# Kernel tuning notes

Hardware: AMD Instinct MI355X
Metric: run time of the kernel (lower is better)

Reference implementation:

```python
import jax, jax.numpy as jnp
import numpy as np

B, DIM, S, CS, H = 1024, 64, 256, 500, 128

def setup_inputs() -> dict:
    key = jax.random.key(0)
    ks = jax.random.split(key, 16)
    def rn(k, shape, scale=0.05):
        return jax.random.normal(k, shape, dtype=jnp.float32) * scale
    return {
        "x": rn(ks[0], (B, DIM, S - 1), 1.0),
        "snippet": jax.random.randint(ks[1], (B, DIM), 0, CS, dtype=jnp.int64),
        "snippet_list": rn(ks[2], (DIM, CS, S), 1.0),
        "W_ih": rn(ks[3], (3 * H, 2 * DIM)),
        "W_hh": rn(ks[4], (3 * H, H)),
        "b_ih": rn(ks[5], (3 * H,)),
        "b_hh": rn(ks[6], (3 * H,)),
        "W1": rn(ks[7], (H // 2, H)),
        "b1": rn(ks[8], (H // 2,)),
        "W2": rn(ks[9], (H // 4, H // 2)),
        "b2": rn(ks[10], (H // 4,)),
        "W3": rn(ks[11], (H // 8, H // 4)),
        "b3": rn(ks[12], (H // 8,)),
        "W_last": rn(ks[13], (DIM, H // 8 + DIM)),
        "b_last": rn(ks[14], (DIM,)),
    }

def _leaky(v):
    return jax.nn.leaky_relu(v, negative_slope=0.01)

def _gru_last(x_seq, W_ih, W_hh, b_ih, b_hh):
    # x_seq: [B, T, I]; returns last hidden state [B, H]
    xg = jnp.einsum('bti,gi->btg', x_seq, W_ih) + b_ih  # [B, T, 3H]
    h0 = jnp.zeros((x_seq.shape[0], H), dtype=x_seq.dtype)
    def step(h, xg_t):
        hg = h @ W_hh.T + b_hh
        xr, xz, xn = jnp.split(xg_t, 3, axis=-1)
        hr, hz, hn = jnp.split(hg, 3, axis=-1)
        r = jax.nn.sigmoid(xr + hr)
        z = jax.nn.sigmoid(xz + hz)
        n = jnp.tanh(xn + r * hn)
        h_new = (1.0 - z) * n + z * h
        return h_new, None
    h_last, _ = jax.lax.scan(step, h0, jnp.swapaxes(xg, 0, 1))
    return h_last

def reference(x, snippet, snippet_list, W_ih, W_hh, b_ih, b_hh,
              W1, b1, W2, b2, W3, b3, W_last, b_last):
    # vectorized gather: snip[b, d, :] = snippet_list[d, snippet[b, d], :]
    snip = snippet_list[jnp.arange(DIM)[None, :], snippet]  # [B, DIM, S]
    last = snip[:, :, -1]          # [B, DIM]
    snip = snip[:, :, :-1]         # [B, DIM, S-1]
    xc = jnp.concatenate((x, snip), axis=1)       # [B, 2*DIM, S-1]
    xc = jnp.swapaxes(xc, 1, 2)                   # [B, S-1, 2*DIM]
    h = _gru_last(xc, W_ih, W_hh, b_ih, b_hh)     # [B, H]
    h = _leaky(h @ W1.T + b1)
    h = _leaky(h @ W2.T + b2)
    h = _leaky(h @ W3.T + b3)
    h = jnp.concatenate((h, last), axis=1)        # [B, H//8 + DIM]
    out = _leaky(h @ W_last.T + b_last)           # [B, DIM]
    return out
```

## Files before the change

kernel.cpp:

```cpp
#include <hip/hip_runtime.h>
#include <hip/hip_bf16.h>

#define B_    1024
#define DIMC  64
#define T_    255
#define H_    128
#define CS_   500
#define S_    256

#define MROWS 16
#define NBLK  (B_ / MROWS)
#define NTHR  512
#define TCH   8
#define XSTR  136

#define OFF_H   69632
#define OFF_IDX 78336
#define SMEMB   82432

typedef __attribute__((ext_vector_type(8))) short bf16x8;
typedef __attribute__((ext_vector_type(4))) float f32x4;

__device__ __forceinline__ unsigned short f2bf(float f) {
    unsigned int u = __builtin_bit_cast(unsigned int, f);
    return (unsigned short)((u + 0x7FFFu + ((u >> 16) & 1u)) >> 16);
}
__device__ __forceinline__ float fast_rcp(float x) { return __builtin_amdgcn_rcpf(x); }
__device__ __forceinline__ float sigm(float x)   { float e = __expf(-x); return fast_rcp(1.0f + e); }
__device__ __forceinline__ float tanh_f(float x) { float e = __expf(2.0f * x); return 1.0f - 2.0f * fast_rcp(1.0f + e); }
__device__ __forceinline__ float leaky(float x)  { return x > 0.0f ? x : 0.01f * x; }
__device__ __forceinline__ int   imin(int a, int b) { return a < b ? a : b; }
__device__ __forceinline__ void bar_lgkm() {
    asm volatile("s_waitcnt lgkmcnt(0)\n\ts_barrier" ::: "memory");
}

#define OW1 0
#define OW2 8256
#define OW3 10336
#define OWL 10864
#define OHF 16048
#define OS1 18096
#define OS2 18608
#define OS3 18864
#define OSL 18992

__global__ __launch_bounds__(NTHR, 2)
void gru_fused(const float* __restrict__ x, const int* __restrict__ snippet,
               const float* __restrict__ slist,
               const float* __restrict__ W_ih, const float* __restrict__ W_hh,
               const float* __restrict__ b_ih, const float* __restrict__ b_hh,
               const float* __restrict__ W1, const float* __restrict__ b1,
               const float* __restrict__ W2, const float* __restrict__ b2,
               const float* __restrict__ W3, const float* __restrict__ b3,
               const float* __restrict__ Wl, const float* __restrict__ bl,
               float* __restrict__ out)
{
    __shared__ __attribute__((aligned(16))) unsigned char smem[SMEMB];
    unsigned short* shx0 = (unsigned short*)smem;
    unsigned short* shh0 = (unsigned short*)(smem + OFF_H);
    int*            sidx = (int*)(smem + OFF_IDX);

    const int tid   = threadIdx.x;
    const int bbase = blockIdx.x * MROWS;
    const int lane  = tid & 63;
    const int wv    = tid >> 6;
    const int l15   = lane & 15;
    const int l4    = lane >> 4;

    for (int i = tid; i < MROWS * DIMC; i += NTHR) {
        int r = i >> 6, d = i & 63;
        sidx[i] = snippet[(bbase + r) * DIMC + d];
    }
    for (int i = tid; i < MROWS * XSTR; i += NTHR) shh0[i] = 0;

    bf16x8 wih[3][4], whh[3][4];
    {
        const int g = (wv << 4) + l15;
#pragma unroll
        for (int gt = 0; gt < 3; ++gt) {
#pragma unroll
            for (int kb = 0; kb < 4; ++kb) {
                const float* p1 = W_ih + (size_t)(gt * 128 + g) * 128 + kb * 32 + (l4 << 3);
                const float* p2 = W_hh + (size_t)(gt * 128 + g) * 128 + kb * 32 + (l4 << 3);
                f32x4 a0, a1, c0, c1;
                __builtin_memcpy(&a0, p1, 16); __builtin_memcpy(&a1, p1 + 4, 16);
                __builtin_memcpy(&c0, p2, 16); __builtin_memcpy(&c1, p2 + 4, 16);
                bf16x8 a, c;
#pragma unroll
                for (int e = 0; e < 4; ++e) {
                    a[e]     = (short)f2bf(a0[e]); a[e + 4] = (short)f2bf(a1[e]);
                    c[e]     = (short)f2bf(c0[e]); c[e + 4] = (short)f2bf(c1[e]);
                }
                wih[gt][kb] = a; whh[gt][kb] = c;
            }
        }
    }
    const int jj = (wv << 4) + l15;
    const float bias_r = b_ih[jj]       + b_hh[jj];
    const float bias_z = b_ih[128 + jj] + b_hh[128 + jj];
    const float bxn    = b_ih[256 + jj];
    const float bhn    = b_hh[256 + jj];

    __syncthreads();

    int rowu[2], k0u[2], isx[2];
    const float* pa[2]; const float* pb[2];
#pragma unroll
    for (int un = 0; un < 2; ++un) {
        int u  = tid + un * NTHR;
        int r  = u >> 6;
        int k0 = (u & 63) << 1;
        rowu[un] = r; k0u[un] = k0;
        if (k0 < DIMC) {
            isx[un] = 1;
            pa[un] = x + ((size_t)(bbase + r) * DIMC + k0) * T_;
            pb[un] = pa[un] + T_;
        } else {
            isx[un] = 0;
            int d = k0 - DIMC;
            pa[un] = slist + ((size_t)d       * CS_ + sidx[(r << 6) + d])     * S_;
            pb[un] = slist + ((size_t)(d + 1) * CS_ + sidx[(r << 6) + d + 1]) * S_;
        }
    }

    f32x4 sa[2][2], sb[2][2];

    auto issue = [&](int t0) {
#pragma unroll
        for (int un = 0; un < 2; ++un) {
            if (isx[un] && t0 + TCH - 1 > T_ - 1) {
#pragma unroll
                for (int g = 0; g < 2; ++g) {
                    f32x4 va, vb;
#pragma unroll
                    for (int e = 0; e < 4; ++e) {
                        int tt = imin(t0 + g * 4 + e, T_ - 1);
                        va[e] = pa[un][tt]; vb[e] = pb[un][tt];
                    }
                    sa[un][g] = va; sb[un][g] = vb;
                }
            } else {
#pragma unroll
                for (int g = 0; g < 2; ++g) {
                    f32x4 va, vb;
                    __builtin_memcpy(&va, pa[un] + t0 + g * 4, 16);
                    __builtin_memcpy(&vb, pb[un] + t0 + g * 4, 16);
                    sa[un][g] = va; sb[un][g] = vb;
                }
            }
        }
    };

    auto commit = [&](int buf) {
        unsigned short* dst = shx0 + buf * (TCH * MROWS * XSTR);
#pragma unroll
        for (int un = 0; un < 2; ++un) {
#pragma unroll
            for (int g = 0; g < 2; ++g) {
#pragma unroll
                for (int e = 0; e < 4; ++e) {
                    int t = g * 4 + e;
                    unsigned pk = (unsigned)f2bf(sa[un][g][e]) | ((unsigned)f2bf(sb[un][g][e]) << 16);
                    *(unsigned*)&dst[(t * MROWS + rowu[un]) * XSTR + k0u[un]] = pk;
                }
            }
        }
    };

    int cur = 0;
    float hprev[4] = {0.f, 0.f, 0.f, 0.f};
    const f32x4 Z = {0.f, 0.f, 0.f, 0.f};

    auto xg_phase = [&](int buf, int tb, int nt, f32x4* xr, f32x4* xz, f32x4* xn) {
        const unsigned short* base = shx0 + buf * (TCH * MROWS * XSTR);
#pragma unroll
        for (int tt = 0; tt < 4; ++tt) {
            if (tt >= nt) break;
            const unsigned short* xp = base + ((tb + tt) * MROWS + l15) * XSTR + (l4 << 3);
            bf16x8 a[4];
#pragma unroll
            for (int kb = 0; kb < 4; ++kb) a[kb] = *(const bf16x8*)(xp + kb * 32);
            f32x4 r = Z, z = Z, n = Z;
#pragma unroll
            for (int kb = 0; kb < 4; ++kb) {
                r = __builtin_amdgcn_mfma_f32_16x16x32_bf16(a[kb], wih[0][kb], r, 0, 0, 0);
                z = __builtin_amdgcn_mfma_f32_16x16x32_bf16(a[kb], wih[1][kb], z, 0, 0, 0);
                n = __builtin_amdgcn_mfma_f32_16x16x32_bf16(a[kb], wih[2][kb], n, 0, 0, 0);
            }
            xr[tt] = r; xz[tt] = z; xn[tt] = n;
        }
    };

    auto recur = [&](f32x4 xr, f32x4 xz, f32x4 xn) {
        const unsigned short* hp = shh0 + cur * (MROWS * XSTR) + l15 * XSTR + (l4 << 3);
        bf16x8 h0 = *(const bf16x8*)(hp);
        bf16x8 h1 = *(const bf16x8*)(hp + 32);
        bf16x8 h2 = *(const bf16x8*)(hp + 64);
        bf16x8 h3 = *(const bf16x8*)(hp + 96);
        f32x4 arA = __builtin_amdgcn_mfma_f32_16x16x32_bf16(h0, whh[0][0], xr, 0, 0, 0);
        f32x4 azA = __builtin_amdgcn_mfma_f32_16x16x32_bf16(h0, whh[1][0], xz, 0, 0, 0);
        f32x4 anA = __builtin_amdgcn_mfma_f32_16x16x32_bf16(h0, whh[2][0], Z,  0, 0, 0);
        f32x4 arB = __builtin_amdgcn_mfma_f32_16x16x32_bf16(h2, whh[0][2], Z,  0, 0, 0);
        f32x4 azB = __builtin_amdgcn_mfma_f32_16x16x32_bf16(h2, whh[1][2], Z,  0, 0, 0);
        f32x4 anB = __builtin_amdgcn_mfma_f32_16x16x32_bf16(h2, whh[2][2], Z,  0, 0, 0);
        arA = __builtin_amdgcn_mfma_f32_16x16x32_bf16(h1, whh[0][1], arA, 0, 0, 0);
        azA = __builtin_amdgcn_mfma_f32_16x16x32_bf16(h1, whh[1][1], azA, 0, 0, 0);
        anA = __builtin_amdgcn_mfma_f32_16x16x32_bf16(h1, whh[2][1], anA, 0, 0, 0);
        arB = __builtin_amdgcn_mfma_f32_16x16x32_bf16(h3, whh[0][3], arB, 0, 0, 0);
        azB = __builtin_amdgcn_mfma_f32_16x16x32_bf16(h3, whh[1][3], azB, 0, 0, 0);
        anB = __builtin_amdgcn_mfma_f32_16x16x32_bf16(h3, whh[2][3], anB, 0, 0, 0);
        unsigned short* hw = shh0 + (cur ^ 1) * (MROWS * XSTR);
#pragma unroll
        for (int q = 0; q < 4; ++q) {
            float r = sigm(arA[q] + arB[q] + bias_r);
            float z = sigm(azA[q] + azB[q] + bias_z);
            float n = tanh_f(xn[q] + bxn + r * (anA[q] + anB[q] + bhn));
            float hn = (1.0f - z) * n + z * hprev[q];
            hprev[q] = hn;
            hw[((l4 << 2) + q) * XSTR + jj] = f2bf(hn);
        }
        bar_lgkm();
        cur ^= 1;
    };

    issue(0);
    commit(0);
    __syncthreads();

    for (int c = 0; c < 31; ++c) {
        issue((c + 1) * TCH);
        const int bx = c & 1;
        f32x4 xr[4], xz[4], xn[4];
        xg_phase(bx, 0, 4, xr, xz, xn);
#pragma unroll
        for (int tt = 0; tt < 4; ++tt) recur(xr[tt], xz[tt], xn[tt]);
        xg_phase(bx, 4, 4, xr, xz, xn);
#pragma unroll
        for (int tt = 0; tt < 4; ++tt) recur(xr[tt], xz[tt], xn[tt]);
        commit((c + 1) & 1);
        bar_lgkm();
    }
    {
        f32x4 xr[4], xz[4], xn[4];
        xg_phase(1, 0, 4, xr, xz, xn);
#pragma unroll
        for (int tt = 0; tt < 4; ++tt) recur(xr[tt], xz[tt], xn[tt]);
        xg_phase(1, 4, 3, xr, xz, xn);
#pragma unroll
        for (int tt = 0; tt < 3; ++tt) recur(xr[tt], xz[tt], xn[tt]);
    }

    float* wl = (float*)smem;

    for (int i = tid; i < 8192; i += NTHR) wl[OW1 + (i >> 7) * 129 + (i & 127)] = W1[i];
    for (int i = tid; i < 2048; i += NTHR) wl[OW2 + (i >> 6) * 65  + (i & 63)]  = W2[i];
    for (int i = tid; i < 512;  i += NTHR) wl[OW3 + (i >> 5) * 33  + (i & 31)]  = W3[i];
    for (int i = tid; i < 5120; i += NTHR) wl[OWL + (i / 80) * 81  + (i % 80)]  = Wl[i];
#pragma unroll
    for (int q = 0; q < 4; ++q) wl[OHF + ((l4 << 2) + q) * 128 + jj] = hprev[q];
    __syncthreads();

    for (int mloc = 0; mloc < 2; ++mloc) {
        const int m = (wv << 1) + mloc;
        {
            float s = b1[lane];
            const float* w = wl + OW1 + lane * 129;
            for (int k = 0; k < 128; ++k) s += wl[OHF + m * 128 + k] * w[k];
            wl[OS1 + wv * 64 + lane] = leaky(s);
        }
        __syncthreads();
        if (lane < 32) {
            float s = b2[lane];
            const float* w = wl + OW2 + lane * 65;
            for (int k = 0; k < 64; ++k) s += wl[OS1 + wv * 64 + k] * w[k];
            wl[OS2 + wv * 32 + lane] = leaky(s);
        } else {
            int d = lane - 32;
            wl[OSL + wv * 64 + d]      = slist[((size_t)d        * CS_ + sidx[(m << 6) + d])      * S_ + (S_ - 1)];
            wl[OSL + wv * 64 + d + 32] = slist[((size_t)(d + 32) * CS_ + sidx[(m << 6) + d + 32]) * S_ + (S_ - 1)];
        }
        __syncthreads();
        if (lane < 16) {
            float s = b3[lane];
            const float* w = wl + OW3 + lane * 33;
            for (int k = 0; k < 32; ++k) s += wl[OS2 + wv * 32 + k] * w[k];
            wl[OS3 + wv * 16 + lane] = leaky(s);
        }
        __syncthreads();
        {
            float s = bl[lane];
            const float* w = wl + OWL + lane * 81;
#pragma unroll
            for (int i = 0; i < 16; ++i) s += wl[OS3 + wv * 16 + i] * w[i];
            for (int d = 0; d < 64; ++d) s += wl[OSL + wv * 64 + d] * w[16 + d];
            out[(size_t)(bbase + m) * DIMC + lane] = leaky(s);
        }
        __syncthreads();
    }
}

extern "C" void kernel_launch(void* const* d_in, const int* in_sizes, int n_in,
                              void* d_out, int out_size, void* d_ws, size_t ws_size,
                              hipStream_t stream) {
    (void)in_sizes; (void)n_in; (void)out_size; (void)d_ws; (void)ws_size;
    const float* x       = (const float*)d_in[0];
    const int*   snippet = (const int*)  d_in[1];
    const float* slist   = (const float*)d_in[2];
    const float* W_ih    = (const float*)d_in[3];
    const float* W_hh    = (const float*)d_in[4];
    const float* b_ih    = (const float*)d_in[5];
    const float* b_hh    = (const float*)d_in[6];
    const float* W1      = (const float*)d_in[7];
    const float* b1      = (const float*)d_in[8];
    const float* W2      = (const float*)d_in[9];
    const float* b2      = (const float*)d_in[10];
    const float* W3      = (const float*)d_in[11];
    const float* b3      = (const float*)d_in[12];
    const float* Wl      = (const float*)d_in[13];
    const float* bl      = (const float*)d_in[14];
    float* out = (float*)d_out;

    hipLaunchKernelGGL(gru_fused, dim3(NBLK), dim3(NTHR), 0, stream,
                       x, snippet, slist, W_ih, W_hh, b_ih, b_hh,
                       W1, b1, W2, b2, W3, b3, Wl, bl, out);
}
```

Measured before the change: 322.4 us.

## Halve block to 4 waves, each owning two 16-column tiles of the GRU

```diff
diff --git a/kernel.cpp b/kernel.cpp
--- a/kernel.cpp
+++ b/kernel.cpp
@@ -10,11 +10,11 @@
 
 #define MROWS 16
 #define NBLK  (B_ / MROWS)
-#define NTHR  512
-#define TCH   8
+#define NTHR  256
+#define TCH   4
 #define XSTR  136
 
-#define OFF_H   69632
+#define OFF_H   34816
 #define OFF_IDX 78336
 #define SMEMB   82432
 
@@ -44,7 +44,7 @@
 #define OS3 18864
 #define OSL 18992
 
-__global__ __launch_bounds__(NTHR, 2)
+__global__ __launch_bounds__(NTHR, 1)
 void gru_fused(const float* __restrict__ x, const int* __restrict__ snippet,
                const float* __restrict__ slist,
                const float* __restrict__ W_ih, const float* __restrict__ W_hh,
@@ -73,80 +73,82 @@
     }
     for (int i = tid; i < MROWS * XSTR; i += NTHR) shh0[i] = 0;
 
-    bf16x8 wih[3][4], whh[3][4];
+    bf16x8 wih[3][2][4], whh[3][2][4];
     {
-        const int g = (wv << 4) + l15;
-#pragma unroll
-        for (int gt = 0; gt < 3; ++gt) {
-#pragma unroll
-            for (int kb = 0; kb < 4; ++kb) {
-                const float* p1 = W_ih + (size_t)(gt * 128 + g) * 128 + kb * 32 + (l4 << 3);
-                const float* p2 = W_hh + (size_t)(gt * 128 + g) * 128 + kb * 32 + (l4 << 3);
-                f32x4 a0, a1, c0, c1;
-                __builtin_memcpy(&a0, p1, 16); __builtin_memcpy(&a1, p1 + 4, 16);
-                __builtin_memcpy(&c0, p2, 16); __builtin_memcpy(&c1, p2 + 4, 16);
-                bf16x8 a, c;
-#pragma unroll
-                for (int e = 0; e < 4; ++e) {
-                    a[e]     = (short)f2bf(a0[e]); a[e + 4] = (short)f2bf(a1[e]);
-                    c[e]     = (short)f2bf(c0[e]); c[e + 4] = (short)f2bf(c1[e]);
+#pragma unroll
+        for (int g = 0; g < 3; ++g) {
+#pragma unroll
+            for (int nt = 0; nt < 2; ++nt) {
+                const int row = g * 128 + (wv << 5) + (nt << 4) + l15;
+#pragma unroll
+                for (int kb = 0; kb < 4; ++kb) {
+                    const float* p1 = W_ih + (size_t)row * 128 + kb * 32 + (l4 << 3);
+                    const float* p2 = W_hh + (size_t)row * 128 + kb * 32 + (l4 << 3);
+                    f32x4 a0, a1, c0, c1;
+                    __builtin_memcpy(&a0, p1, 16); __builtin_memcpy(&a1, p1 + 4, 16);
+                    __builtin_memcpy(&c0, p2, 16); __builtin_memcpy(&c1, p2 + 4, 16);
+                    bf16x8 a, c;
+#pragma unroll
+                    for (int e = 0; e < 4; ++e) {
+                        a[e] = (short)f2bf(a0[e]); a[e + 4] = (short)f2bf(a1[e]);
+                        c[e] = (short)f2bf(c0[e]); c[e + 4] = (short)f2bf(c1[e]);
+                    }
+                    wih[g][nt][kb] = a; whh[g][nt][kb] = c;
                 }
-                wih[gt][kb] = a; whh[gt][kb] = c;
-            }
-        }
-    }
-    const int jj = (wv << 4) + l15;
-    const float bias_r = b_ih[jj]       + b_hh[jj];
-    const float bias_z = b_ih[128 + jj] + b_hh[128 + jj];
-    const float bxn    = b_ih[256 + jj];
-    const float bhn    = b_hh[256 + jj];
+            }
+        }
+    }
+    float biasR[2], biasZ[2], biasXN[2], biasHN[2];
+#pragma unroll
+    for (int nt = 0; nt < 2; ++nt) {
+        int col = (wv << 5) + (nt << 4) + l15;
+        biasR[nt]  = b_ih[col]       + b_hh[col];
+        biasZ[nt]  = b_ih[128 + col] + b_hh[128 + col];
+        biasXN[nt] = b_ih[256 + col];
+        biasHN[nt] = b_hh[256 + col];
+    }
 
     __syncthreads();
 
-    int rowu[2], k0u[2], isx[2];
-    const float* pa[2]; const float* pb[2];
-#pragma unroll
-    for (int un = 0; un < 2; ++un) {
-        int u  = tid + un * NTHR;
-        int r  = u >> 6;
-        int k0 = (u & 63) << 1;
-        rowu[un] = r; k0u[un] = k0;
-        if (k0 < DIMC) {
-            isx[un] = 1;
+    const int k0   = (tid & 63) << 1;
+    const int isx  = (k0 < DIMC);
+    const float* pa[4]; const float* pb[4];
+    int rowu[4];
+#pragma unroll
+    for (int un = 0; un < 4; ++un) {
+        int r = (tid >> 6) + (un << 2);
+        rowu[un] = r;
+        if (isx) {
             pa[un] = x + ((size_t)(bbase + r) * DIMC + k0) * T_;
             pb[un] = pa[un] + T_;
         } else {
-            isx[un] = 0;
             int d = k0 - DIMC;
             pa[un] = slist + ((size_t)d       * CS_ + sidx[(r << 6) + d])     * S_;
             pb[un] = slist + ((size_t)(d + 1) * CS_ + sidx[(r << 6) + d + 1]) * S_;
         }
     }
 
-    f32x4 sa[2][2], sb[2][2];
+    f32x4 sa[4], sb[4];
 
     auto issue = [&](int t0) {
-#pragma unroll
-        for (int un = 0; un < 2; ++un) {
-            if (isx[un] && t0 + TCH - 1 > T_ - 1) {
-#pragma unroll
-                for (int g = 0; g < 2; ++g) {
-                    f32x4 va, vb;
-#pragma unroll
-                    for (int e = 0; e < 4; ++e) {
-                        int tt = imin(t0 + g * 4 + e, T_ - 1);
-                        va[e] = pa[un][tt]; vb[e] = pb[un][tt];
-                    }
-                    sa[un][g] = va; sb[un][g] = vb;
+        if (isx && t0 + TCH - 1 > T_ - 1) {
+#pragma unroll
+            for (int un = 0; un < 4; ++un) {
+                f32x4 va, vb;
+#pragma unroll
+                for (int e = 0; e < 4; ++e) {
+                    int tt = imin(t0 + e, T_ - 1);
+                    va[e] = pa[un][tt]; vb[e] = pb[un][tt];
                 }
-            } else {
-#pragma unroll
-                for (int g = 0; g < 2; ++g) {
-                    f32x4 va, vb;
-                    __builtin_memcpy(&va, pa[un] + t0 + g * 4, 16);
-                    __builtin_memcpy(&vb, pb[un] + t0 + g * 4, 16);
-                    sa[un][g] = va; sb[un][g] = vb;
-                }
+                sa[un] = va; sb[un] = vb;
+            }
+        } else {
+#pragma unroll
+            for (int un = 0; un < 4; ++un) {
+                f32x4 va, vb;
+                __builtin_memcpy(&va, pa[un] + t0, 16);
+                __builtin_memcpy(&vb, pb[un] + t0, 16);
+                sa[un] = va; sb[un] = vb;
             }
         }
     };
@@ -154,70 +156,77 @@
     auto commit = [&](int buf) {
         unsigned short* dst = shx0 + buf * (TCH * MROWS * XSTR);
 #pragma unroll
-        for (int un = 0; un < 2; ++un) {
-#pragma unroll
-            for (int g = 0; g < 2; ++g) {
-#pragma unroll
-                for (int e = 0; e < 4; ++e) {
-                    int t = g * 4 + e;
-                    unsigned pk = (unsigned)f2bf(sa[un][g][e]) | ((unsigned)f2bf(sb[un][g][e]) << 16);
-                    *(unsigned*)&dst[(t * MROWS + rowu[un]) * XSTR + k0u[un]] = pk;
-                }
+        for (int un = 0; un < 4; ++un) {
+#pragma unroll
+            for (int e = 0; e < 4; ++e) {
+                unsigned pk = (unsigned)f2bf(sa[un][e]) | ((unsigned)f2bf(sb[un][e]) << 16);
+                *(unsigned*)&dst[(e * MROWS + rowu[un]) * XSTR + k0] = pk;
             }
         }
     };
 
     int cur = 0;
-    float hprev[4] = {0.f, 0.f, 0.f, 0.f};
+    float hprev[8] = {0.f};
     const f32x4 Z = {0.f, 0.f, 0.f, 0.f};
 
-    auto xg_phase = [&](int buf, int tb, int nt, f32x4* xr, f32x4* xz, f32x4* xn) {
+    f32x4 xg[2][3][2];
+
+    auto xg2 = [&](int buf, int tb, int nsteps) {
         const unsigned short* base = shx0 + buf * (TCH * MROWS * XSTR);
 #pragma unroll
-        for (int tt = 0; tt < 4; ++tt) {
-            if (tt >= nt) break;
+        for (int tt = 0; tt < 2; ++tt) {
+            if (tt >= nsteps) break;
             const unsigned short* xp = base + ((tb + tt) * MROWS + l15) * XSTR + (l4 << 3);
             bf16x8 a[4];
 #pragma unroll
             for (int kb = 0; kb < 4; ++kb) a[kb] = *(const bf16x8*)(xp + kb * 32);
-            f32x4 r = Z, z = Z, n = Z;
-#pragma unroll
-            for (int kb = 0; kb < 4; ++kb) {
-                r = __builtin_amdgcn_mfma_f32_16x16x32_bf16(a[kb], wih[0][kb], r, 0, 0, 0);
-                z = __builtin_amdgcn_mfma_f32_16x16x32_bf16(a[kb], wih[1][kb], z, 0, 0, 0);
-                n = __builtin_amdgcn_mfma_f32_16x16x32_bf16(a[kb], wih[2][kb], n, 0, 0, 0);
-            }
-            xr[tt] = r; xz[tt] = z; xn[tt] = n;
+#pragma unroll
+            for (int nt = 0; nt < 2; ++nt) {
+                f32x4 r = {biasR[nt],  biasR[nt],  biasR[nt],  biasR[nt]};
+                f32x4 z = {biasZ[nt],  biasZ[nt],  biasZ[nt],  biasZ[nt]};
+                f32x4 n = {biasXN[nt], biasXN[nt], biasXN[nt], biasXN[nt]};
+#pragma unroll
+                for (int kb = 0; kb < 4; ++kb) {
+                    r = __builtin_amdgcn_mfma_f32_16x16x32_bf16(a[kb], wih[0][nt][kb], r, 0, 0, 0);
+                    z = __builtin_amdgcn_mfma_f32_16x16x32_bf16(a[kb], wih[1][nt][kb], z, 0, 0, 0);
+                    n = __builtin_amdgcn_mfma_f32_16x16x32_bf16(a[kb], wih[2][nt][kb], n, 0, 0, 0);
+                }
+                xg[tt][0][nt] = r; xg[tt][1][nt] = z; xg[tt][2][nt] = n;
+            }
         }
     };
 
-    auto recur = [&](f32x4 xr, f32x4 xz, f32x4 xn) {
+    auto recur = [&](int st) {
         const unsigned short* hp = shh0 + cur * (MROWS * XSTR) + l15 * XSTR + (l4 << 3);
         bf16x8 h0 = *(const bf16x8*)(hp);
         bf16x8 h1 = *(const bf16x8*)(hp + 32);
         bf16x8 h2 = *(const bf16x8*)(hp + 64);
         bf16x8 h3 = *(const bf16x8*)(hp + 96);
-        f32x4 arA = __builtin_amdgcn_mfma_f32_16x16x32_bf16(h0, whh[0][0], xr, 0, 0, 0);
-        f32x4 azA = __builtin_amdgcn_mfma_f32_16x16x32_bf16(h0, whh[1][0], xz, 0, 0, 0);
-        f32x4 anA = __builtin_amdgcn_mfma_f32_16x16x32_bf16(h0, whh[2][0], Z,  0, 0, 0);
-        f32x4 arB = __builtin_amdgcn_mfma_f32_16x16x32_bf16(h2, whh[0][2], Z,  0, 0, 0);
-        f32x4 azB = __builtin_amdgcn_mfma_f32_16x16x32_bf16(h2, whh[1][2], Z,  0, 0, 0);
-        f32x4 anB = __builtin_amdgcn_mfma_f32_16x16x32_bf16(h2, whh[2][2], Z,  0, 0, 0);
-        arA = __builtin_amdgcn_mfma_f32_16x16x32_bf16(h1, whh[0][1], arA, 0, 0, 0);
-        azA = __builtin_amdgcn_mfma_f32_16x16x32_bf16(h1, whh[1][1], azA, 0, 0, 0);
-        anA = __builtin_amdgcn_mfma_f32_16x16x32_bf16(h1, whh[2][1], anA, 0, 0, 0);
-        arB = __builtin_amdgcn_mfma_f32_16x16x32_bf16(h3, whh[0][3], arB, 0, 0, 0);
-        azB = __builtin_amdgcn_mfma_f32_16x16x32_bf16(h3, whh[1][3], azB, 0, 0, 0);
-        anB = __builtin_amdgcn_mfma_f32_16x16x32_bf16(h3, whh[2][3], anB, 0, 0, 0);
         unsigned short* hw = shh0 + (cur ^ 1) * (MROWS * XSTR);
 #pragma unroll
-        for (int q = 0; q < 4; ++q) {
-            float r = sigm(arA[q] + arB[q] + bias_r);
-            float z = sigm(azA[q] + azB[q] + bias_z);
-            float n = tanh_f(xn[q] + bxn + r * (anA[q] + anB[q] + bhn));
-            float hn = (1.0f - z) * n + z * hprev[q];
-            hprev[q] = hn;
-            hw[((l4 << 2) + q) * XSTR + jj] = f2bf(hn);
+        for (int nt = 0; nt < 2; ++nt) {
+            f32x4 seedN = {biasHN[nt], biasHN[nt], biasHN[nt], biasHN[nt]};
+            f32x4 rA = __builtin_amdgcn_mfma_f32_16x16x32_bf16(h0, whh[0][nt][0], xg[st][0][nt], 0, 0, 0);
+            f32x4 zA = __builtin_amdgcn_mfma_f32_16x16x32_bf16(h0, whh[1][nt][0], xg[st][1][nt], 0, 0, 0);
+            f32x4 nA = __builtin_amdgcn_mfma_f32_16x16x32_bf16(h0, whh[2][nt][0], seedN, 0, 0, 0);
+            f32x4 rB = __builtin_amdgcn_mfma_f32_16x16x32_bf16(h2, whh[0][nt][2], Z, 0, 0, 0);
+            f32x4 zB = __builtin_amdgcn_mfma_f32_16x16x32_bf16(h2, whh[1][nt][2], Z, 0, 0, 0);
+            f32x4 nB = __builtin_amdgcn_mfma_f32_16x16x32_bf16(h2, whh[2][nt][2], Z, 0, 0, 0);
+            rA = __builtin_amdgcn_mfma_f32_16x16x32_bf16(h1, whh[0][nt][1], rA, 0, 0, 0);
+            zA = __builtin_amdgcn_mfma_f32_16x16x32_bf16(h1, whh[1][nt][1], zA, 0, 0, 0);
+            nA = __builtin_amdgcn_mfma_f32_16x16x32_bf16(h1, whh[2][nt][1], nA, 0, 0, 0);
+            rB = __builtin_amdgcn_mfma_f32_16x16x32_bf16(h3, whh[0][nt][3], rB, 0, 0, 0);
+            zB = __builtin_amdgcn_mfma_f32_16x16x32_bf16(h3, whh[1][nt][3], zB, 0, 0, 0);
+            nB = __builtin_amdgcn_mfma_f32_16x16x32_bf16(h3, whh[2][nt][3], nB, 0, 0, 0);
+#pragma unroll
+            for (int q = 0; q < 4; ++q) {
+                float r  = sigm(rA[q] + rB[q]);
+                float z  = sigm(zA[q] + zB[q]);
+                float n  = tanh_f(xg[st][2][nt][q] + r * (nA[q] + nB[q]));
+                float hn = n + z * (hprev[nt * 4 + q] - n);
+                hprev[nt * 4 + q] = hn;
+                hw[((l4 << 2) + q) * XSTR + (wv << 5) + (nt << 4) + l15] = f2bf(hn);
+            }
         }
         bar_lgkm();
         cur ^= 1;
@@ -227,28 +236,20 @@
     commit(0);
     __syncthreads();
 
-    for (int c = 0; c < 31; ++c) {
+    for (int c = 0; c < 63; ++c) {
         issue((c + 1) * TCH);
         const int bx = c & 1;
-        f32x4 xr[4], xz[4], xn[4];
-        xg_phase(bx, 0, 4, xr, xz, xn);
-#pragma unroll
-        for (int tt = 0; tt < 4; ++tt) recur(xr[tt], xz[tt], xn[tt]);
-        xg_phase(bx, 4, 4, xr, xz, xn);
-#pragma unroll
-        for (int tt = 0; tt < 4; ++tt) recur(xr[tt], xz[tt], xn[tt]);
+        xg2(bx, 0, 2);
+        recur(0); recur(1);
+        xg2(bx, 2, 2);
+        recur(0); recur(1);
         commit((c + 1) & 1);
         bar_lgkm();
     }
-    {
-        f32x4 xr[4], xz[4], xn[4];
-        xg_phase(1, 0, 4, xr, xz, xn);
-#pragma unroll
-        for (int tt = 0; tt < 4; ++tt) recur(xr[tt], xz[tt], xn[tt]);
-        xg_phase(1, 4, 3, xr, xz, xn);
-#pragma unroll
-        for (int tt = 0; tt < 3; ++tt) recur(xr[tt], xz[tt], xn[tt]);
-    }
+    xg2(1, 0, 2);
+    recur(0); recur(1);
+    xg2(1, 2, 1);
+    recur(0);
 
     float* wl = (float*)smem;
 
@@ -257,11 +258,14 @@
     for (int i = tid; i < 512;  i += NTHR) wl[OW3 + (i >> 5) * 33  + (i & 31)]  = W3[i];
     for (int i = tid; i < 5120; i += NTHR) wl[OWL + (i / 80) * 81  + (i % 80)]  = Wl[i];
 #pragma unroll
-    for (int q = 0; q < 4; ++q) wl[OHF + ((l4 << 2) + q) * 128 + jj] = hprev[q];
+    for (int nt = 0; nt < 2; ++nt)
+#pragma unroll
+        for (int q = 0; q < 4; ++q)
+            wl[OHF + ((l4 << 2) + q) * 128 + (wv << 5) + (nt << 4) + l15] = hprev[nt * 4 + q];
     __syncthreads();
 
-    for (int mloc = 0; mloc < 2; ++mloc) {
-        const int m = (wv << 1) + mloc;
+    for (int mloc = 0; mloc < 4; ++mloc) {
+        const int m = (wv << 2) + mloc;
         {
             float s = b1[lane];
             const float* w = wl + OW1 + lane * 129;
```

After: 372.5 us. 1.16x slower.

## Pre-scale GRU weights by log2e, transpose MFMA operands, fold biases into accumulators

Applied to the files above, without the earlier changes.

```diff
diff --git a/kernel.cpp b/kernel.cpp
--- a/kernel.cpp
+++ b/kernel.cpp
@@ -12,22 +12,32 @@
 #define NBLK  (B_ / MROWS)
 #define NTHR  512
 #define TCH   8
-#define XSTR  136
-
-#define OFF_H   69632
-#define OFF_IDX 78336
-#define SMEMB   82432
+#define XSX   152
+#define XSH   152
+#define HSZ   (MROWS * XSH)
+
+#define OFF_H   77824
+#define OFF_IDX 87552
+#define SMEMB   91648
 
 typedef __attribute__((ext_vector_type(8))) short bf16x8;
 typedef __attribute__((ext_vector_type(4))) float f32x4;
+
+#define LOG2E 1.4426950408889634f
 
 __device__ __forceinline__ unsigned short f2bf(float f) {
     unsigned int u = __builtin_bit_cast(unsigned int, f);
     return (unsigned short)((u + 0x7FFFu + ((u >> 16) & 1u)) >> 16);
 }
 __device__ __forceinline__ float fast_rcp(float x) { return __builtin_amdgcn_rcpf(x); }
-__device__ __forceinline__ float sigm(float x)   { float e = __expf(-x); return fast_rcp(1.0f + e); }
-__device__ __forceinline__ float tanh_f(float x) { float e = __expf(2.0f * x); return 1.0f - 2.0f * fast_rcp(1.0f + e); }
+#if __has_builtin(__builtin_amdgcn_exp2f)
+__device__ __forceinline__ float EXP2(float x) { return __builtin_amdgcn_exp2f(x); }
+#else
+__device__ __forceinline__ float EXP2(float x) { float r; asm("v_exp_f32 %0, %1" : "=v"(r) : "v"(x)); return r; }
+#endif
+__device__ __forceinline__ unsigned cvt_pk_bf16(float lo, float hi) {
+    unsigned r; asm("v_cvt_pk_bf16_f32 %0, %1, %2" : "=v"(r) : "v"(lo), "v"(hi)); return r;
+}
 __device__ __forceinline__ float leaky(float x)  { return x > 0.0f ? x : 0.01f * x; }
 __device__ __forceinline__ int   imin(int a, int b) { return a < b ? a : b; }
 __device__ __forceinline__ void bar_lgkm() {
@@ -56,8 +66,8 @@
                float* __restrict__ out)
 {
     __shared__ __attribute__((aligned(16))) unsigned char smem[SMEMB];
-    unsigned short* shx0 = (unsigned short*)smem;
-    unsigned short* shh0 = (unsigned short*)(smem + OFF_H);
+    unsigned short* shx = (unsigned short*)smem;
+    unsigned short* shh = (unsigned short*)(smem + OFF_H);
     int*            sidx = (int*)(smem + OFF_IDX);
 
     const int tid   = threadIdx.x;
@@ -71,11 +81,12 @@
         int r = i >> 6, d = i & 63;
         sidx[i] = snippet[(bbase + r) * DIMC + d];
     }
-    for (int i = tid; i < MROWS * XSTR; i += NTHR) shh0[i] = 0;
+    for (int i = tid; i < 2 * HSZ; i += NTHR) shh[i] = 0;
 
     bf16x8 wih[3][4], whh[3][4];
     {
         const int g = (wv << 4) + l15;
+        const float sc[3] = { -LOG2E, -LOG2E, 2.0f * LOG2E };
 #pragma unroll
         for (int gt = 0; gt < 3; ++gt) {
 #pragma unroll
@@ -88,18 +99,23 @@
                 bf16x8 a, c;
 #pragma unroll
                 for (int e = 0; e < 4; ++e) {
-                    a[e]     = (short)f2bf(a0[e]); a[e + 4] = (short)f2bf(a1[e]);
-                    c[e]     = (short)f2bf(c0[e]); c[e + 4] = (short)f2bf(c1[e]);
+                    a[e] = (short)f2bf(a0[e] * sc[gt]); a[e + 4] = (short)f2bf(a1[e] * sc[gt]);
+                    c[e] = (short)f2bf(c0[e] * sc[gt]); c[e + 4] = (short)f2bf(c1[e] * sc[gt]);
                 }
                 wih[gt][kb] = a; whh[gt][kb] = c;
             }
         }
     }
-    const int jj = (wv << 4) + l15;
-    const float bias_r = b_ih[jj]       + b_hh[jj];
-    const float bias_z = b_ih[128 + jj] + b_hh[128 + jj];
-    const float bxn    = b_ih[256 + jj];
-    const float bhn    = b_hh[256 + jj];
+    const int c0col = (wv << 4) + (l4 << 2);
+    f32x4 biasR4, biasZ4, biasXN4, biasHN4;
+#pragma unroll
+    for (int q = 0; q < 4; ++q) {
+        int col = c0col + q;
+        biasR4[q]  = (b_ih[col]       + b_hh[col])       * (-LOG2E);
+        biasZ4[q]  = (b_ih[128 + col] + b_hh[128 + col]) * (-LOG2E);
+        biasXN4[q] = b_ih[256 + col] * (2.0f * LOG2E);
+        biasHN4[q] = b_hh[256 + col] * (2.0f * LOG2E);
+    }
 
     __syncthreads();
 
@@ -152,7 +168,7 @@
     };
 
     auto commit = [&](int buf) {
-        unsigned short* dst = shx0 + buf * (TCH * MROWS * XSTR);
+        unsigned short* dst = shx + buf * (TCH * MROWS * XSX);
 #pragma unroll
         for (int un = 0; un < 2; ++un) {
 #pragma unroll
@@ -160,8 +176,8 @@
 #pragma unroll
                 for (int e = 0; e < 4; ++e) {
                     int t = g * 4 + e;
-                    unsigned pk = (unsigned)f2bf(sa[un][g][e]) | ((unsigned)f2bf(sb[un][g][e]) << 16);
-                    *(unsigned*)&dst[(t * MROWS + rowu[un]) * XSTR + k0u[un]] = pk;
+                    unsigned pk = cvt_pk_bf16(sa[un][g][e], sb[un][g][e]);
+                    *(unsigned*)&dst[(t * MROWS + rowu[un]) * XSX + k0u[un]] = pk;
                 }
             }
         }
@@ -171,54 +187,60 @@
     float hprev[4] = {0.f, 0.f, 0.f, 0.f};
     const f32x4 Z = {0.f, 0.f, 0.f, 0.f};
 
-    auto xg_phase = [&](int buf, int tb, int nt, f32x4* xr, f32x4* xz, f32x4* xn) {
-        const unsigned short* base = shx0 + buf * (TCH * MROWS * XSTR);
-#pragma unroll
-        for (int tt = 0; tt < 4; ++tt) {
+    f32x4 xg[2][3];
+
+    auto xg2 = [&](int buf, int tb, int nt) {
+        const unsigned short* base = shx + buf * (TCH * MROWS * XSX);
+#pragma unroll
+        for (int tt = 0; tt < 2; ++tt) {
             if (tt >= nt) break;
-            const unsigned short* xp = base + ((tb + tt) * MROWS + l15) * XSTR + (l4 << 3);
+            const unsigned short* xp = base + ((tb + tt) * MROWS + l15) * XSX + (l4 << 3);
             bf16x8 a[4];
 #pragma unroll
             for (int kb = 0; kb < 4; ++kb) a[kb] = *(const bf16x8*)(xp + kb * 32);
-            f32x4 r = Z, z = Z, n = Z;
+            f32x4 r = biasR4, z = biasZ4, n = biasXN4;
 #pragma unroll
             for (int kb = 0; kb < 4; ++kb) {
-                r = __builtin_amdgcn_mfma_f32_16x16x32_bf16(a[kb], wih[0][kb], r, 0, 0, 0);
-                z = __builtin_amdgcn_mfma_f32_16x16x32_bf16(a[kb], wih[1][kb], z, 0, 0, 0);
-                n = __builtin_amdgcn_mfma_f32_16x16x32_bf16(a[kb], wih[2][kb], n, 0, 0, 0);
+                r = __builtin_amdgcn_mfma_f32_16x16x32_bf16(wih[0][kb], a[kb], r, 0, 0, 0);
+                z = __builtin_amdgcn_mfma_f32_16x16x32_bf16(wih[1][kb], a[kb], z, 0, 0, 0);
+                n = __builtin_amdgcn_mfma_f32_16x16x32_bf16(wih[2][kb], a[kb], n, 0, 0, 0);
             }
-            xr[tt] = r; xz[tt] = z; xn[tt] = n;
+            xg[tt][0] = r; xg[tt][1] = z; xg[tt][2] = n;
         }
     };
 
-    auto recur = [&](f32x4 xr, f32x4 xz, f32x4 xn) {
-        const unsigned short* hp = shh0 + cur * (MROWS * XSTR) + l15 * XSTR + (l4 << 3);
+    auto recur = [&](int st) {
+        const unsigned short* hp = shh + cur * HSZ + l15 * XSH + (l4 << 3);
         bf16x8 h0 = *(const bf16x8*)(hp);
         bf16x8 h1 = *(const bf16x8*)(hp + 32);
         bf16x8 h2 = *(const bf16x8*)(hp + 64);
         bf16x8 h3 = *(const bf16x8*)(hp + 96);
-        f32x4 arA = __builtin_amdgcn_mfma_f32_16x16x32_bf16(h0, whh[0][0], xr, 0, 0, 0);
-        f32x4 azA = __builtin_amdgcn_mfma_f32_16x16x32_bf16(h0, whh[1][0], xz, 0, 0, 0);
-        f32x4 anA = __builtin_amdgcn_mfma_f32_16x16x32_bf16(h0, whh[2][0], Z,  0, 0, 0);
-        f32x4 arB = __builtin_amdgcn_mfma_f32_16x16x32_bf16(h2, whh[0][2], Z,  0, 0, 0);
-        f32x4 azB = __builtin_amdgcn_mfma_f32_16x16x32_bf16(h2, whh[1][2], Z,  0, 0, 0);
-        f32x4 anB = __builtin_amdgcn_mfma_f32_16x16x32_bf16(h2, whh[2][2], Z,  0, 0, 0);
-        arA = __builtin_amdgcn_mfma_f32_16x16x32_bf16(h1, whh[0][1], arA, 0, 0, 0);
-        azA = __builtin_amdgcn_mfma_f32_16x16x32_bf16(h1, whh[1][1], azA, 0, 0, 0);
-        anA = __builtin_amdgcn_mfma_f32_16x16x32_bf16(h1, whh[2][1], anA, 0, 0, 0);
-        arB = __builtin_amdgcn_mfma_f32_16x16x32_bf16(h3, whh[0][3], arB, 0, 0, 0);
-        azB = __builtin_amdgcn_mfma_f32_16x16x32_bf16(h3, whh[1][3], azB, 0, 0, 0);
-        anB = __builtin_amdgcn_mfma_f32_16x16x32_bf16(h3, whh[2][3], anB, 0, 0, 0);
-        unsigned short* hw = shh0 + (cur ^ 1) * (MROWS * XSTR);
+        f32x4 arA = __builtin_amdgcn_mfma_f32_16x16x32_bf16(whh[0][0], h0, xg[st][0], 0, 0, 0);
+        f32x4 azA = __builtin_amdgcn_mfma_f32_16x16x32_bf16(whh[1][0], h0, xg[st][1], 0, 0, 0);
+        f32x4 anA = __builtin_amdgcn_mfma_f32_16x16x32_bf16(whh[2][0], h0, biasHN4,   0, 0, 0);
+        f32x4 arB = __builtin_amdgcn_mfma_f32_16x16x32_bf16(whh[0][2], h2, Z, 0, 0, 0);
+        f32x4 azB = __builtin_amdgcn_mfma_f32_16x16x32_bf16(whh[1][2], h2, Z, 0, 0, 0);
+        f32x4 anB = __builtin_amdgcn_mfma_f32_16x16x32_bf16(whh[2][2], h2, Z, 0, 0, 0);
+        arA = __builtin_amdgcn_mfma_f32_16x16x32_bf16(whh[0][1], h1, arA, 0, 0, 0);
+        azA = __builtin_amdgcn_mfma_f32_16x16x32_bf16(whh[1][1], h1, azA, 0, 0, 0);
+        anA = __builtin_amdgcn_mfma_f32_16x16x32_bf16(whh[2][1], h1, anA, 0, 0, 0);
+        arB = __builtin_amdgcn_mfma_f32_16x16x32_bf16(whh[0][3], h3, arB, 0, 0, 0);
+        azB = __builtin_amdgcn_mfma_f32_16x16x32_bf16(whh[1][3], h3, azB, 0, 0, 0);
+        anB = __builtin_amdgcn_mfma_f32_16x16x32_bf16(whh[2][3], h3, anB, 0, 0, 0);
+        float hn[4];
 #pragma unroll
         for (int q = 0; q < 4; ++q) {
-            float r = sigm(arA[q] + arB[q] + bias_r);
-            float z = sigm(azA[q] + azB[q] + bias_z);
-            float n = tanh_f(xn[q] + bxn + r * (anA[q] + anB[q] + bhn));
-            float hn = (1.0f - z) * n + z * hprev[q];
-            hprev[q] = hn;
-            hw[((l4 << 2) + q) * XSTR + jj] = f2bf(hn);
-        }
+            float r    = fast_rcp(1.0f + EXP2(arA[q] + arB[q]));
+            float z    = fast_rcp(1.0f + EXP2(azA[q] + azB[q]));
+            float narg = __builtin_fmaf(r, anA[q] + anB[q], xg[st][2][q]);
+            float tn   = __builtin_fmaf(-2.0f, fast_rcp(1.0f + EXP2(narg)), 1.0f);
+            hn[q] = __builtin_fmaf(z, hprev[q] - tn, tn);
+            hprev[q] = hn[q];
+        }
+        unsigned p0 = cvt_pk_bf16(hn[0], hn[1]);
+        unsigned p1 = cvt_pk_bf16(hn[2], hn[3]);
+        unsigned long long pk = (unsigned long long)p0 | ((unsigned long long)p1 << 32);
+        *(unsigned long long*)&shh[(cur ^ 1) * HSZ + l15 * XSH + c0col] = pk;
         bar_lgkm();
         cur ^= 1;
     };
@@ -230,25 +252,18 @@
     for (int c = 0; c < 31; ++c) {
         issue((c + 1) * TCH);
         const int bx = c & 1;
-        f32x4 xr[4], xz[4], xn[4];
-        xg_phase(bx, 0, 4, xr, xz, xn);
-#pragma unroll
-        for (int tt = 0; tt < 4; ++tt) recur(xr[tt], xz[tt], xn[tt]);
-        xg_phase(bx, 4, 4, xr, xz, xn);
-#pragma unroll
-        for (int tt = 0; tt < 4; ++tt) recur(xr[tt], xz[tt], xn[tt]);
+#pragma unroll
+        for (int sb = 0; sb < 4; ++sb) {
+            xg2(bx, sb * 2, 2);
+            recur(0); recur(1);
+        }
         commit((c + 1) & 1);
         bar_lgkm();
     }
-    {
-        f32x4 xr[4], xz[4], xn[4];
-        xg_phase(1, 0, 4, xr, xz, xn);
-#pragma unroll
-        for (int tt = 0; tt < 4; ++tt) recur(xr[tt], xz[tt], xn[tt]);
-        xg_phase(1, 4, 3, xr, xz, xn);
-#pragma unroll
-        for (int tt = 0; tt < 3; ++tt) recur(xr[tt], xz[tt], xn[tt]);
-    }
+    xg2(1, 0, 2); recur(0); recur(1);
+    xg2(1, 2, 2); recur(0); recur(1);
+    xg2(1, 4, 2); recur(0); recur(1);
+    xg2(1, 6, 1); recur(0);
 
     float* wl = (float*)smem;
 
@@ -257,7 +272,8 @@
     for (int i = tid; i < 512;  i += NTHR) wl[OW3 + (i >> 5) * 33  + (i & 31)]  = W3[i];
     for (int i = tid; i < 5120; i += NTHR) wl[OWL + (i / 80) * 81  + (i % 80)]  = Wl[i];
 #pragma unroll
-    for (int q = 0; q < 4; ++q) wl[OHF + ((l4 << 2) + q) * 128 + jj] = hprev[q];
+    for (int q = 0; q < 4; ++q)
+        wl[OHF + l15 * 128 + c0col + q] = hprev[q];
     __syncthreads();
 
     for (int mloc = 0; mloc < 2; ++mloc) {
```

After: 337.5 us. 1.05x slower.
